# Kernel optimization log

Measured on AMD Instinct MI355X. Metric: run time of the kernel, lower is better.

## Reference

```python
import jax, jax.numpy as jnp
import numpy as np

B, QT, KT = 4, 1024, 1024
Q_SIZE, K_SIZE, EMB, HEADS = 1024, 1024, 1024, 8
HEAD_DIM = EMB // HEADS


def setup_inputs() -> dict:
    key = jax.random.key(0)
    ks = jax.random.split(key, 8)
    query = jax.random.normal(ks[0], (B, QT, Q_SIZE), dtype=jnp.float32)
    key_t = jax.random.normal(ks[1], (B, KT, K_SIZE), dtype=jnp.float32)
    mask = jax.random.randint(ks[2], (B, QT, KT), 0, 2, dtype=jnp.int32)
    # Linear weights stored as (in, out); torch Linear computes x @ W.T, equivalent here.
    sq = 1.0 / np.sqrt(Q_SIZE)
    sk = 1.0 / np.sqrt(K_SIZE)
    se = 1.0 / np.sqrt(EMB)
    Wq = jax.random.uniform(ks[3], (Q_SIZE, EMB), jnp.float32, -sq, sq)
    Wk = jax.random.uniform(ks[4], (K_SIZE, EMB), jnp.float32, -sk, sk)
    Wv = jax.random.uniform(ks[5], (K_SIZE, EMB), jnp.float32, -sk, sk)
    Wu = jax.random.uniform(ks[6], (EMB, EMB), jnp.float32, -se, se)
    bu = jax.random.uniform(ks[7], (EMB,), jnp.float32, -se, se)
    return {"query": query, "key": key_t, "mask": mask,
            "Wq": Wq, "Wk": Wk, "Wv": Wv, "Wu": Wu, "bu": bu}


def reference(query, key, mask, Wq, Wk, Wv, Wu, bu):
    b, q_t, _ = query.shape
    k_t = key.shape[1]
    q = (query @ Wq).reshape(b, q_t, HEADS, HEAD_DIM)   # b i n d
    k = (key @ Wk).reshape(b, k_t, HEADS, HEAD_DIM)     # b j n d
    v = (key @ Wv).reshape(b, k_t, HEADS, HEAD_DIM)
    # NOTE: original module defines self.scale but never applies it.
    att_score = jnp.einsum('bind,bjnd->bijn', q, k)
    att_score = jnp.where(mask[..., None] == 0, jnp.float32(-1e9), att_score)
    att_prob = jax.nn.softmax(att_score, axis=2)        # softmax over key axis j
    att_vec = jnp.einsum('bijn,bjnd->bind', att_prob, v).reshape(b, q_t, EMB)
    return att_vec @ Wu + bu
```

## Files before the change

kernel.cpp:

```cpp
#include <hip/hip_runtime.h>
#include <hip/hip_bf16.h>


typedef __attribute__((ext_vector_type(8))) short bf16x8;
typedef __attribute__((ext_vector_type(4))) float f32x4;

static constexpr int BB = 4;
static constexpr int TT = 1024;
static constexpr int EE = 1024;
static constexpr int HH = 8;
static constexpr int DD = 128;

static __device__ __forceinline__ unsigned short f2b(float x) {
  union { float f; unsigned int u; } c; c.f = x;
  unsigned int r = c.u + 0x7fffu + ((c.u >> 16) & 1u);
  return (unsigned short)(r >> 16);
}

static __device__ __forceinline__ unsigned int cvtpk(float lo, float hi) {
  unsigned int r;
  asm("v_cvt_pk_bf16_f32 %0, %1, %2" : "=v"(r) : "v"(lo), "v"(hi));
  return r;
}

static __device__ __forceinline__ float exp2x(float x) {
  float r;
  asm("v_exp_f32 %0, %1" : "=v"(r) : "v"(x));
  return r;
}

static __device__ __forceinline__ void gload_lds16(const void* g, void* l) {
  __builtin_amdgcn_global_load_lds(
      (const __attribute__((address_space(1))) unsigned int*)g,
      (__attribute__((address_space(3))) unsigned int*)l, 16, 0, 0);
}

__global__ __launch_bounds__(256) void cvt_kernel(
    const float* __restrict__ qf, const float* __restrict__ kf,
    unsigned short* __restrict__ qb, unsigned short* __restrict__ kb) {
  int i = blockIdx.x * 256 + threadIdx.x;
  float4 a = ((const float4*)qf)[i];
  ushort4 oa; oa.x = f2b(a.x); oa.y = f2b(a.y); oa.z = f2b(a.z); oa.w = f2b(a.w);
  ((ushort4*)qb)[i] = oa;
  float4 b = ((const float4*)kf)[i];
  ushort4 ob; ob.x = f2b(b.x); ob.y = f2b(b.y); ob.z = f2b(b.z); ob.w = f2b(b.w);
  ((ushort4*)kb)[i] = ob;
}

struct WT4 { const float* src[4]; unsigned short* dst[4]; float scale[4]; };

__global__ __launch_bounds__(256) void wtrans_kernel(WT4 wt) {
  const float* src = wt.src[blockIdx.z];
  unsigned short* dst = wt.dst[blockIdx.z];
  const float sc = wt.scale[blockIdx.z];
  __shared__ float tile[32][33];
  int n0 = blockIdx.x * 32, k0 = blockIdx.y * 32;
  int tx = threadIdx.x, ty = threadIdx.y;
#pragma unroll
  for (int i = 0; i < 4; ++i)
    tile[ty + i * 8][tx] = src[(size_t)(k0 + ty + i * 8) * EE + n0 + tx];
  __syncthreads();
#pragma unroll
  for (int i = 0; i < 4; ++i)
    dst[(size_t)(n0 + ty + i * 8) * EE + k0 + tx] = f2b(tile[tx][ty + i * 8] * sc);
}

__global__ __launch_bounds__(256) void vtrans_kernel(
    const unsigned short* __restrict__ vp, unsigned short* __restrict__ vt) {
  int bh = blockIdx.z; int b = bh >> 3, h = bh & 7;
  int d0 = blockIdx.x * 32, kt0 = blockIdx.y * 32;
  __shared__ unsigned short tile[32][33];
  int tx = threadIdx.x, ty = threadIdx.y;
#pragma unroll
  for (int i = 0; i < 4; ++i)
    tile[ty + i * 8][tx] =
        vp[(size_t)(b * TT + kt0 + ty + i * 8) * EE + h * DD + d0 + tx];
  __syncthreads();
#pragma unroll
  for (int i = 0; i < 4; ++i)
    vt[(size_t)((b * HH + h) * DD + d0 + ty + i * 8) * TT + kt0 + tx] =
        tile[tx][ty + i * 8];
}

__global__ __launch_bounds__(256) void maskpack_kernel(
    const int* __restrict__ mask, unsigned long long* __restrict__ mbits) {
  int row = blockIdx.x * 4 + (threadIdx.x >> 6);
  int lane = threadIdx.x & 63;
  const int* mrow = mask + (size_t)row * TT;
  unsigned long long myw = 0;
#pragma unroll
  for (int jw = 0; jw < 16; ++jw) {
    unsigned long long bal = __ballot(mrow[jw * 64 + lane] != 0);
    if (lane == jw) myw = bal;
  }
  if (lane < 16) mbits[(size_t)row * 16 + lane] = myw;
}

static __device__ __forceinline__ void gemm_core(
    const unsigned short* __restrict__ A, const unsigned short* __restrict__ Bt,
    unsigned short* __restrict__ Cb) {
  constexpr int K = EE, N = EE;
  __shared__ __align__(16) unsigned short As[128 * 32];
  __shared__ __align__(16) unsigned short Bs[128 * 32];
  const int tid = threadIdx.x, lane = tid & 63, w = tid >> 6;
  const int wm = w >> 1, wn = w & 1;
  const int bm = blockIdx.x, bn = blockIdx.y;
  const int g4 = lane >> 4, l15 = lane & 15;
  const int srow = lane >> 2;
  const int scol = (lane & 3) * 8;

  f32x4 acc[4][4] = {};

  for (int kt = 0; kt < K / 32; ++kt) {
    const int k0 = kt * 32;
#pragma unroll
    for (int it = 0; it < 2; ++it) {
      int r = it * 64 + w * 16;
      gload_lds16(A + (size_t)(bm * 128 + r + srow) * K + k0 + scol, As + r * 32);
      gload_lds16(Bt + (size_t)(bn * 128 + r + srow) * K + k0 + scol, Bs + r * 32);
    }
    __syncthreads();
    bf16x8 af[4], bf[4];
#pragma unroll
    for (int i = 0; i < 4; ++i) {
      af[i] = *(const bf16x8*)(As + (wm * 64 + i * 16 + l15) * 32 + g4 * 8);
      bf[i] = *(const bf16x8*)(Bs + (wn * 64 + i * 16 + l15) * 32 + g4 * 8);
    }
#pragma unroll
    for (int i = 0; i < 4; ++i)
#pragma unroll
      for (int j = 0; j < 4; ++j)
        acc[i][j] = __builtin_amdgcn_mfma_f32_16x16x32_bf16(af[i], bf[j],
                                                            acc[i][j], 0, 0, 0);
    __syncthreads();
  }

  const int rr = g4 * 4;
#pragma unroll
  for (int i = 0; i < 4; ++i)
#pragma unroll
    for (int j = 0; j < 4; ++j) {
      int row = bm * 128 + wm * 64 + i * 16 + rr;
      int col = bn * 128 + wn * 64 + j * 16 + l15;
#pragma unroll
      for (int r = 0; r < 4; ++r)
        Cb[(size_t)(row + r) * N + col] = f2b(acc[i][j][r]);
    }
}

struct Gemm3 { const unsigned short* A[3]; const unsigned short* Bt[3];
               unsigned short* C[3]; };

__global__ __launch_bounds__(256) void proj_gemm_kernel(Gemm3 g) {
  int z = blockIdx.z;
  gemm_core(g.A[z], g.Bt[z], g.C[z]);
}

__global__ __launch_bounds__(256) void out_gemm_kernel(
    const unsigned short* __restrict__ A, const unsigned short* __restrict__ Bt,
    float* __restrict__ Cf, const float* __restrict__ bias) {
  constexpr int K = EE, N = EE;
  __shared__ __align__(16) unsigned short As[64 * 32];
  __shared__ __align__(16) unsigned short Bs[128 * 32];
  const int tid = threadIdx.x, lane = tid & 63, w = tid >> 6;
  const int wm = w >> 1, wn = w & 1;
  const int bm = blockIdx.x, bn = blockIdx.y;
  const int g4 = lane >> 4, l15 = lane & 15;

  f32x4 acc[2][4] = {};

  for (int kt = 0; kt < K / 32; ++kt) {
    const int k0 = kt * 32;
    {
      int row = tid >> 2, c = tid & 3;
      gload_lds16(A + (size_t)(bm * 64 + row) * K + k0 + c * 8, As + tid * 8);
    }
#pragma unroll
    for (int it = 0; it < 2; ++it) {
      int idx = it * 256 + tid;
      int row = idx >> 2, c = idx & 3;
      gload_lds16(Bt + (size_t)(bn * 128 + row) * K + k0 + c * 8, Bs + idx * 8);
    }
    __syncthreads();
    bf16x8 af[2], bf[4];
#pragma unroll
    for (int i = 0; i < 2; ++i)
      af[i] = *(const bf16x8*)(As + (wm * 32 + i * 16 + l15) * 32 + g4 * 8);
#pragma unroll
    for (int j = 0; j < 4; ++j)
      bf[j] = *(const bf16x8*)(Bs + (wn * 64 + j * 16 + l15) * 32 + g4 * 8);
#pragma unroll
    for (int i = 0; i < 2; ++i)
#pragma unroll
      for (int j = 0; j < 4; ++j)
        acc[i][j] = __builtin_amdgcn_mfma_f32_16x16x32_bf16(af[i], bf[j],
                                                            acc[i][j], 0, 0, 0);
    __syncthreads();
  }

  const int rr = g4 * 4;
#pragma unroll
  for (int i = 0; i < 2; ++i)
#pragma unroll
    for (int j = 0; j < 4; ++j) {
      int row = bm * 64 + wm * 32 + i * 16 + rr;
      int col = bn * 128 + wn * 64 + j * 16 + l15;
#pragma unroll
      for (int r = 0; r < 4; ++r)
        Cf[(size_t)(row + r) * N + col] = acc[i][j][r] + bias[col];
    }
}

__global__ __launch_bounds__(256) void attn_kernel(
    const unsigned short* __restrict__ q, const unsigned short* __restrict__ k,
    const unsigned short* __restrict__ vt,
    const unsigned long long* __restrict__ mbits,
    unsigned short* __restrict__ av) {
  extern __shared__ __align__(16) char smem[];

  const int tid = threadIdx.x, lane = tid & 63, w = tid >> 6;
  const int orig = blockIdx.x + 16 * blockIdx.y + 128 * blockIdx.z;
  const int qt = (orig >> 3) & 15;
  const int pair = ((orig & 7) << 2) | (orig >> 7);
  const int h = pair & 7, b = pair >> 3;
  const int i0 = qt * 64 + w * 16;
  const int g4 = lane >> 4, l15 = lane & 15;
  const int swz = (l15 & 7) << 4;

  bf16x8 aq[4];
  {
    const unsigned short* qb =
        q + (size_t)(b * TT + i0 + l15) * EE + h * DD + g4 * 8;
#pragma unroll
    for (int kc = 0; kc < 4; ++kc) aq[kc] = *(const bf16x8*)(qb + kc * 32);
  }

  const unsigned short* kb0 = k + (size_t)(b * TT) * EE + h * DD;
  const unsigned short* vb0 = vt + (size_t)((b * HH + h) * DD) * TT;
  const unsigned short* kptr[4];
  const unsigned short* vptr[4];
  int chunkb[4];
#pragma unroll
  for (int p = 0; p < 4; ++p) {
    int base = p * 256 + w * 64;
    int idx = base + lane;
    int kr = idx >> 4, kcc = (idx & 15) ^ (kr & 7);
    kptr[p] = kb0 + (size_t)kr * EE + kcc * 8;
    int vr = idx >> 3, vcc = (idx & 7) ^ (vr & 7);
    vptr[p] = vb0 + (size_t)vr * TT + vcc * 8;
    chunkb[p] = base * 16;
  }

  const unsigned long long* mb = mbits + ((size_t)(b * TT + i0 + l15) << 4);
  unsigned long long mcur = mb[0];

  int kb_[4], vb_[2];
#pragma unroll
  for (int kc = 0; kc < 4; ++kc)
    kb_[kc] = l15 * 256 + ((kc * 64 + g4 * 16) ^ swz);
#pragma unroll
  for (int h2 = 0; h2 < 2; ++h2)
    vb_[h2] = 32768 + l15 * 128 + ((h2 * 64 + g4 * 16) ^ swz);

#pragma unroll
  for (int p = 0; p < 4; ++p) {
    gload_lds16(kptr[p], smem + chunkb[p]);
    gload_lds16(vptr[p], smem + 32768 + chunkb[p]);
  }
#pragma unroll
  for (int p = 0; p < 4; ++p) { kptr[p] += 64 * EE; vptr[p] += 64; }

  f32x4 oacc[8] = {};
  float mrun = -__builtin_inff(), lrun = 0.f;

  __syncthreads();
  int bufoff = 0;

  for (int t = 0; t < 16; ++t) {
    unsigned long long mnext = 0;
    if (t < 15) {
      mnext = mb[t + 1];
      int dst = bufoff ^ 16384;
#pragma unroll
      for (int p = 0; p < 4; ++p) {
        gload_lds16(kptr[p], smem + dst + chunkb[p]);
        gload_lds16(vptr[p], smem + 32768 + dst + chunkb[p]);
      }
#pragma unroll
      for (int p = 0; p < 4; ++p) { kptr[p] += 64 * EE; vptr[p] += 64; }
    }

    f32x4 sacc[4] = {};
    __builtin_amdgcn_s_setprio(1);
#pragma unroll
    for (int kc = 0; kc < 4; ++kc)
#pragma unroll
      for (int nt = 0; nt < 4; ++nt) {
        bf16x8 bk = *(const bf16x8*)(smem + kb_[kc] + nt * 4096);
        sacc[nt] = __builtin_amdgcn_mfma_f32_16x16x32_bf16(bk, aq[kc],
                                                           sacc[nt], 0, 0, 0);
      }
    __builtin_amdgcn_s_setprio(0);

    {
      unsigned int wlo = (unsigned int)mcur, whi = (unsigned int)(mcur >> 32);
#pragma unroll
      for (int nt = 0; nt < 4; ++nt) {
        unsigned int ww = (nt < 2) ? wlo : whi;
        int bb = (nt & 1) * 16 + g4 * 4;
#pragma unroll
        for (int r = 0; r < 4; ++r)
          if (((ww >> (bb + r)) & 1u) == 0u) sacc[nt][r] = -1e9f;
      }
    }

    float mx = sacc[0][0];
#pragma unroll
    for (int nt = 0; nt < 4; ++nt)
#pragma unroll
      for (int r = 0; r < 4; ++r) mx = fmaxf(mx, sacc[nt][r]);
    mx = fmaxf(mx, __shfl_xor(mx, 16, 64));
    mx = fmaxf(mx, __shfl_xor(mx, 32, 64));

    if (__any(mx > mrun + 8.f)) {
      float mnew = fmaxf(mrun, mx);
      float sc = exp2x(mrun - mnew);
      lrun *= sc;
      mrun = mnew;
      float scO[4];
#pragma unroll
      for (int r = 0; r < 4; ++r)
        scO[r] = __shfl(sc, (lane & 48) | (((lane & 48) >> 2) + r), 64);
#pragma unroll
      for (int dt = 0; dt < 8; ++dt)
#pragma unroll
        for (int r = 0; r < 4; ++r) oacc[dt][r] *= scO[r];
    }

    float p[4][4];
    float s0 = 0.f;
#pragma unroll
    for (int nt = 0; nt < 4; ++nt)
#pragma unroll
      for (int r = 0; r < 4; ++r) {
        float pv = exp2x(sacc[nt][r] - mrun);
        p[nt][r] = pv;
        s0 += pv;
      }
    s0 += __shfl_xor(s0, 16, 64);
    s0 += __shfl_xor(s0, 32, 64);
    lrun += s0;

    unsigned int paw[2][4];
#pragma unroll
    for (int h2 = 0; h2 < 2; ++h2) {
      unsigned int D0a = cvtpk(p[2 * h2][0], p[2 * h2][1]);
      unsigned int D1a = cvtpk(p[2 * h2][2], p[2 * h2][3]);
      unsigned int D0b = cvtpk(p[2 * h2 + 1][0], p[2 * h2 + 1][1]);
      unsigned int D1b = cvtpk(p[2 * h2 + 1][2], p[2 * h2 + 1][3]);
      unsigned int r1 = __shfl_xor(g4 < 2 ? D0a : D0b, 16, 64);
      unsigned int r2 = __shfl_xor(g4 < 2 ? D1a : D1b, 16, 64);
      unsigned int r3 = __shfl_xor(g4 == 0 ? D0b : D0a, 32, 64);
      unsigned int r4 = __shfl_xor(g4 == 0 ? D1b : D1a, 32, 64);
      unsigned int r5 = __shfl_xor(g4 == 2 ? D0a : D0b, 48, 64);
      unsigned int r6 = __shfl_xor(g4 == 2 ? D1a : D1b, 48, 64);
      paw[h2][0] = g4 == 0 ? D0a : g4 == 1 ? r5 : g4 == 2 ? r3 : r1;
      paw[h2][1] = g4 == 0 ? D1a : g4 == 1 ? r6 : g4 == 2 ? r4 : r2;
      paw[h2][2] = g4 == 0 ? r1 : g4 == 1 ? r3 : g4 == 2 ? r5 : D0b;
      paw[h2][3] = g4 == 0 ? r2 : g4 == 1 ? r4 : g4 == 2 ? r6 : D1b;
    }

    __builtin_amdgcn_s_setprio(1);
#pragma unroll
    for (int h2 = 0; h2 < 2; ++h2) {
      union { unsigned int u[4]; bf16x8 v; } pau;
      pau.u[0] = paw[h2][0]; pau.u[1] = paw[h2][1];
      pau.u[2] = paw[h2][2]; pau.u[3] = paw[h2][3];
#pragma unroll
      for (int dt = 0; dt < 8; ++dt) {
        bf16x8 bv = *(const bf16x8*)(smem + vb_[h2] + dt * 2048);
        oacc[dt] = __builtin_amdgcn_mfma_f32_16x16x32_bf16(pau.v, bv, oacc[dt],
                                                           0, 0, 0);
      }
    }
    __builtin_amdgcn_s_setprio(0);

    __syncthreads();
    bufoff ^= 16384;
#pragma unroll
    for (int kc = 0; kc < 4; ++kc) kb_[kc] ^= 16384;
#pragma unroll
    for (int h2 = 0; h2 < 2; ++h2) vb_[h2] ^= 16384;
    mcur = mnext;
  }

  float linv[4];
#pragma unroll
  for (int r = 0; r < 4; ++r)
    linv[r] = 1.f / __shfl(lrun, (lane & 48) | (((lane & 48) >> 2) + r), 64);
  unsigned short* ob =
      av + (size_t)(b * TT + i0 + g4 * 4) * EE + h * DD + l15;
#pragma unroll
  for (int dt = 0; dt < 8; ++dt)
#pragma unroll
    for (int r = 0; r < 4; ++r)
      ob[(size_t)r * EE + dt * 16] = f2b(oacc[dt][r] * linv[r]);
}

extern "C" void kernel_launch(void* const* d_in, const int* in_sizes, int n_in,
                              void* d_out, int out_size, void* d_ws,
                              size_t ws_size, hipStream_t stream) {
  const float* query = (const float*)d_in[0];
  const float* key   = (const float*)d_in[1];
  const int*   mask  = (const int*)d_in[2];
  const float* Wq    = (const float*)d_in[3];
  const float* Wk    = (const float*)d_in[4];
  const float* Wv    = (const float*)d_in[5];
  const float* Wu    = (const float*)d_in[6];
  const float* bu    = (const float*)d_in[7];
  float* out = (float*)d_out;

  char* ws = (char*)d_ws;
  const size_t MB = 1024 * 1024;
  unsigned short* qbf = (unsigned short*)(ws);
  unsigned short* kbf = (unsigned short*)(ws + 8 * MB);
  unsigned short* Wqt = (unsigned short*)(ws + 16 * MB);
  unsigned short* Wkt = (unsigned short*)(ws + 18 * MB);
  unsigned short* Wvt = (unsigned short*)(ws + 20 * MB);
  unsigned short* Wut = (unsigned short*)(ws + 22 * MB);
  unsigned short* qp  = (unsigned short*)(ws + 24 * MB);
  unsigned short* kp  = (unsigned short*)(ws + 32 * MB);
  unsigned short* vp  = (unsigned short*)(ws + 40 * MB);
  unsigned short* vtb = (unsigned short*)(ws + 48 * MB);
  unsigned short* av  = (unsigned short*)(ws + 56 * MB);
  unsigned long long* mbt = (unsigned long long*)(ws + 40 * MB);

  cvt_kernel<<<4096, 256, 0, stream>>>(query, key, qbf, kbf);

  WT4 wt; wt.src[0] = Wq; wt.src[1] = Wk; wt.src[2] = Wv; wt.src[3] = Wu;
  wt.dst[0] = Wqt; wt.dst[1] = Wkt; wt.dst[2] = Wvt; wt.dst[3] = Wut;
  wt.scale[0] = 1.4426950408889634f;
  wt.scale[1] = 1.0f; wt.scale[2] = 1.0f; wt.scale[3] = 1.0f;
  wtrans_kernel<<<dim3(32, 32, 4), dim3(32, 8), 0, stream>>>(wt);

  Gemm3 g3;
  g3.A[0] = qbf; g3.A[1] = kbf; g3.A[2] = kbf;
  g3.Bt[0] = Wqt; g3.Bt[1] = Wkt; g3.Bt[2] = Wvt;
  g3.C[0] = qp; g3.C[1] = kp; g3.C[2] = vp;
  proj_gemm_kernel<<<dim3(32, 8, 3), 256, 0, stream>>>(g3);

  vtrans_kernel<<<dim3(4, 32, 32), dim3(32, 8), 0, stream>>>(vp, vtb);

  maskpack_kernel<<<1024, 256, 0, stream>>>(mask, mbt);

  attn_kernel<<<dim3(16, 8, 4), 256, 65536, stream>>>(qp, kp, vtb, mbt, av);

  out_gemm_kernel<<<dim3(64, 8), 256, 0, stream>>>(av, Wut, out, bu);
}
```

Measured before the change: 119.4 us.

## Load V fragments directly to registers in attention; widen projection GEMM K-tile with swizzle

The attention kernel stops staging V through shared memory. Each wave now loads its V^T MFMA operands straight from global memory into registers at the start of every key tile. This halves the dynamic LDS to 32 KB and adds a launch-bounds hint of 2 blocks per CU for higher occupancy, at the cost of more VGPRs and uncoalesced, redundantly fetched global V loads. Separately, the projection GEMM moves to a 64-wide K tile with an XOR-swizzled LDS layout, which halves the barrier count and reduces bank conflicts.

```diff
diff --git a/kernel.cpp b/kernel.cpp
--- a/kernel.cpp
+++ b/kernel.cpp
@@ -100,38 +100,43 @@
     const unsigned short* __restrict__ A, const unsigned short* __restrict__ Bt,
     unsigned short* __restrict__ Cb) {
   constexpr int K = EE, N = EE;
-  __shared__ __align__(16) unsigned short As[128 * 32];
-  __shared__ __align__(16) unsigned short Bs[128 * 32];
+  __shared__ __align__(16) unsigned short As[128 * 64];
+  __shared__ __align__(16) unsigned short Bs[128 * 64];
   const int tid = threadIdx.x, lane = tid & 63, w = tid >> 6;
   const int wm = w >> 1, wn = w & 1;
   const int bm = blockIdx.x, bn = blockIdx.y;
   const int g4 = lane >> 4, l15 = lane & 15;
-  const int srow = lane >> 2;
-  const int scol = (lane & 3) * 8;
 
   f32x4 acc[4][4] = {};
 
-  for (int kt = 0; kt < K / 32; ++kt) {
-    const int k0 = kt * 32;
-#pragma unroll
-    for (int it = 0; it < 2; ++it) {
-      int r = it * 64 + w * 16;
-      gload_lds16(A + (size_t)(bm * 128 + r + srow) * K + k0 + scol, As + r * 32);
-      gload_lds16(Bt + (size_t)(bn * 128 + r + srow) * K + k0 + scol, Bs + r * 32);
+  for (int kt = 0; kt < K / 64; ++kt) {
+    const int k0 = kt * 64;
+#pragma unroll
+    for (int it = 0; it < 4; ++it) {
+      int idx = it * 256 + tid;
+      int r = idx >> 3, c = (idx & 7) ^ (r & 7);
+      gload_lds16(A + (size_t)(bm * 128 + r) * K + k0 + c * 8, As + idx * 8);
+      gload_lds16(Bt + (size_t)(bn * 128 + r) * K + k0 + c * 8, Bs + idx * 8);
     }
     __syncthreads();
-    bf16x8 af[4], bf[4];
-#pragma unroll
-    for (int i = 0; i < 4; ++i) {
-      af[i] = *(const bf16x8*)(As + (wm * 64 + i * 16 + l15) * 32 + g4 * 8);
-      bf[i] = *(const bf16x8*)(Bs + (wn * 64 + i * 16 + l15) * 32 + g4 * 8);
-    }
-#pragma unroll
-    for (int i = 0; i < 4; ++i)
-#pragma unroll
-      for (int j = 0; j < 4; ++j)
-        acc[i][j] = __builtin_amdgcn_mfma_f32_16x16x32_bf16(af[i], bf[j],
-                                                            acc[i][j], 0, 0, 0);
+    bf16x8 af[2][4], bf[2][4];
+#pragma unroll
+    for (int kc2 = 0; kc2 < 2; ++kc2) {
+      int co = ((kc2 * 4 + g4) ^ (l15 & 7)) * 8;
+#pragma unroll
+      for (int i = 0; i < 4; ++i) {
+        af[kc2][i] = *(const bf16x8*)(As + (wm * 64 + i * 16 + l15) * 64 + co);
+        bf[kc2][i] = *(const bf16x8*)(Bs + (wn * 64 + i * 16 + l15) * 64 + co);
+      }
+    }
+#pragma unroll
+    for (int kc2 = 0; kc2 < 2; ++kc2)
+#pragma unroll
+      for (int i = 0; i < 4; ++i)
+#pragma unroll
+        for (int j = 0; j < 4; ++j)
+          acc[i][j] = __builtin_amdgcn_mfma_f32_16x16x32_bf16(
+              af[kc2][i], bf[kc2][j], acc[i][j], 0, 0, 0);
     __syncthreads();
   }
 
@@ -211,7 +216,7 @@
     }
 }
 
-__global__ __launch_bounds__(256) void attn_kernel(
+__global__ __launch_bounds__(256, 2) void attn_kernel(
     const unsigned short* __restrict__ q, const unsigned short* __restrict__ k,
     const unsigned short* __restrict__ vt,
     const unsigned long long* __restrict__ mbits,
@@ -236,9 +241,7 @@
   }
 
   const unsigned short* kb0 = k + (size_t)(b * TT) * EE + h * DD;
-  const unsigned short* vb0 = vt + (size_t)((b * HH + h) * DD) * TT;
   const unsigned short* kptr[4];
-  const unsigned short* vptr[4];
   int chunkb[4];
 #pragma unroll
   for (int p = 0; p < 4; ++p) {
@@ -246,29 +249,24 @@
     int idx = base + lane;
     int kr = idx >> 4, kcc = (idx & 15) ^ (kr & 7);
     kptr[p] = kb0 + (size_t)kr * EE + kcc * 8;
-    int vr = idx >> 3, vcc = (idx & 7) ^ (vr & 7);
-    vptr[p] = vb0 + (size_t)vr * TT + vcc * 8;
     chunkb[p] = base * 16;
   }
+
+  const unsigned short* vfb =
+      vt + (size_t)((b * HH + h) * DD + l15) * TT + g4 * 8;
 
   const unsigned long long* mb = mbits + ((size_t)(b * TT + i0 + l15) << 4);
   unsigned long long mcur = mb[0];
 
-  int kb_[4], vb_[2];
+  int kb_[4];
 #pragma unroll
   for (int kc = 0; kc < 4; ++kc)
     kb_[kc] = l15 * 256 + ((kc * 64 + g4 * 16) ^ swz);
-#pragma unroll
-  for (int h2 = 0; h2 < 2; ++h2)
-    vb_[h2] = 32768 + l15 * 128 + ((h2 * 64 + g4 * 16) ^ swz);
-
-#pragma unroll
-  for (int p = 0; p < 4; ++p) {
-    gload_lds16(kptr[p], smem + chunkb[p]);
-    gload_lds16(vptr[p], smem + 32768 + chunkb[p]);
-  }
-#pragma unroll
-  for (int p = 0; p < 4; ++p) { kptr[p] += 64 * EE; vptr[p] += 64; }
+
+#pragma unroll
+  for (int p = 0; p < 4; ++p) gload_lds16(kptr[p], smem + chunkb[p]);
+#pragma unroll
+  for (int p = 0; p < 4; ++p) kptr[p] += 64 * EE;
 
   f32x4 oacc[8] = {};
   float mrun = -__builtin_inff(), lrun = 0.f;
@@ -277,17 +275,26 @@
   int bufoff = 0;
 
   for (int t = 0; t < 16; ++t) {
+    bf16x8 vr[2][8];
+    {
+      const unsigned short* vtt = vfb + t * 64;
+#pragma unroll
+      for (int h2 = 0; h2 < 2; ++h2)
+#pragma unroll
+        for (int dt = 0; dt < 8; ++dt)
+          vr[h2][dt] =
+              *(const bf16x8*)(vtt + (size_t)dt * 16 * TT + h2 * 32);
+    }
+
     unsigned long long mnext = 0;
     if (t < 15) {
       mnext = mb[t + 1];
       int dst = bufoff ^ 16384;
 #pragma unroll
-      for (int p = 0; p < 4; ++p) {
+      for (int p = 0; p < 4; ++p)
         gload_lds16(kptr[p], smem + dst + chunkb[p]);
-        gload_lds16(vptr[p], smem + 32768 + dst + chunkb[p]);
-      }
-#pragma unroll
-      for (int p = 0; p < 4; ++p) { kptr[p] += 64 * EE; vptr[p] += 64; }
+#pragma unroll
+      for (int p = 0; p < 4; ++p) kptr[p] += 64 * EE;
     }
 
     f32x4 sacc[4] = {};
@@ -377,11 +384,9 @@
       pau.u[0] = paw[h2][0]; pau.u[1] = paw[h2][1];
       pau.u[2] = paw[h2][2]; pau.u[3] = paw[h2][3];
 #pragma unroll
-      for (int dt = 0; dt < 8; ++dt) {
-        bf16x8 bv = *(const bf16x8*)(smem + vb_[h2] + dt * 2048);
-        oacc[dt] = __builtin_amdgcn_mfma_f32_16x16x32_bf16(pau.v, bv, oacc[dt],
-                                                           0, 0, 0);
-      }
+      for (int dt = 0; dt < 8; ++dt)
+        oacc[dt] = __builtin_amdgcn_mfma_f32_16x16x32_bf16(
+            pau.v, vr[h2][dt], oacc[dt], 0, 0, 0);
     }
     __builtin_amdgcn_s_setprio(0);
 
@@ -389,8 +394,6 @@
     bufoff ^= 16384;
 #pragma unroll
     for (int kc = 0; kc < 4; ++kc) kb_[kc] ^= 16384;
-#pragma unroll
-    for (int h2 = 0; h2 < 2; ++h2) vb_[h2] ^= 16384;
     mcur = mnext;
   }
 
@@ -453,7 +456,7 @@
 
   maskpack_kernel<<<1024, 256, 0, stream>>>(mask, mbt);
 
-  attn_kernel<<<dim3(16, 8, 4), 256, 65536, stream>>>(qp, kp, vtb, mbt, av);
+  attn_kernel<<<dim3(16, 8, 4), 256, 32768, stream>>>(qp, kp, vtb, mbt, av);
 
   out_gemm_kernel<<<dim3(64, 8), 256, 0, stream>>>(av, Wut, out, bu);
 }
```

Result: slower. 151.2 us (+26.6%).

## Deepen GEMM K-tile with XOR swizzle and relax attention loop barrier placement

Applied to the files above, without the earlier changes.

The projection GEMM now stages 64-wide K tiles instead of 32, halving the number of barrier pairs per K loop. It uses an XOR-swizzled LDS layout so the wider rows do not cause bank conflicts on the fragment reads. In the attention loop, the end-of-iteration __syncthreads is replaced by a bare s_barrier at the start of the next iteration plus an explicit vmcnt wait that lets the prefetch of the next K/V tile stay in flight. The hand-written waitcnt/barrier ordering is fragile: if the vmcnt count does not match the number of outstanding loads, data races on the double buffer could appear.

```diff
diff --git a/kernel.cpp b/kernel.cpp
--- a/kernel.cpp
+++ b/kernel.cpp
@@ -100,38 +100,43 @@
     const unsigned short* __restrict__ A, const unsigned short* __restrict__ Bt,
     unsigned short* __restrict__ Cb) {
   constexpr int K = EE, N = EE;
-  __shared__ __align__(16) unsigned short As[128 * 32];
-  __shared__ __align__(16) unsigned short Bs[128 * 32];
+  __shared__ __align__(16) unsigned short As[128 * 64];
+  __shared__ __align__(16) unsigned short Bs[128 * 64];
   const int tid = threadIdx.x, lane = tid & 63, w = tid >> 6;
   const int wm = w >> 1, wn = w & 1;
   const int bm = blockIdx.x, bn = blockIdx.y;
   const int g4 = lane >> 4, l15 = lane & 15;
-  const int srow = lane >> 2;
-  const int scol = (lane & 3) * 8;
 
   f32x4 acc[4][4] = {};
 
-  for (int kt = 0; kt < K / 32; ++kt) {
-    const int k0 = kt * 32;
-#pragma unroll
-    for (int it = 0; it < 2; ++it) {
-      int r = it * 64 + w * 16;
-      gload_lds16(A + (size_t)(bm * 128 + r + srow) * K + k0 + scol, As + r * 32);
-      gload_lds16(Bt + (size_t)(bn * 128 + r + srow) * K + k0 + scol, Bs + r * 32);
+  for (int kt = 0; kt < K / 64; ++kt) {
+    const int k0 = kt * 64;
+#pragma unroll
+    for (int it = 0; it < 4; ++it) {
+      int idx = it * 256 + tid;
+      int r = idx >> 3, c = (idx & 7) ^ (r & 7);
+      gload_lds16(A + (size_t)(bm * 128 + r) * K + k0 + c * 8, As + idx * 8);
+      gload_lds16(Bt + (size_t)(bn * 128 + r) * K + k0 + c * 8, Bs + idx * 8);
     }
     __syncthreads();
-    bf16x8 af[4], bf[4];
-#pragma unroll
-    for (int i = 0; i < 4; ++i) {
-      af[i] = *(const bf16x8*)(As + (wm * 64 + i * 16 + l15) * 32 + g4 * 8);
-      bf[i] = *(const bf16x8*)(Bs + (wn * 64 + i * 16 + l15) * 32 + g4 * 8);
-    }
-#pragma unroll
-    for (int i = 0; i < 4; ++i)
-#pragma unroll
-      for (int j = 0; j < 4; ++j)
-        acc[i][j] = __builtin_amdgcn_mfma_f32_16x16x32_bf16(af[i], bf[j],
-                                                            acc[i][j], 0, 0, 0);
+    bf16x8 af[2][4], bf[2][4];
+#pragma unroll
+    for (int kc2 = 0; kc2 < 2; ++kc2) {
+      int co = ((kc2 * 4 + g4) ^ (l15 & 7)) * 8;
+#pragma unroll
+      for (int i = 0; i < 4; ++i) {
+        af[kc2][i] = *(const bf16x8*)(As + (wm * 64 + i * 16 + l15) * 64 + co);
+        bf[kc2][i] = *(const bf16x8*)(Bs + (wn * 64 + i * 16 + l15) * 64 + co);
+      }
+    }
+#pragma unroll
+    for (int kc2 = 0; kc2 < 2; ++kc2)
+#pragma unroll
+      for (int i = 0; i < 4; ++i)
+#pragma unroll
+        for (int j = 0; j < 4; ++j)
+          acc[i][j] = __builtin_amdgcn_mfma_f32_16x16x32_bf16(
+              af[kc2][i], bf[kc2][j], acc[i][j], 0, 0, 0);
     __syncthreads();
   }
 
@@ -277,6 +282,8 @@
   int bufoff = 0;
 
   for (int t = 0; t < 16; ++t) {
+    if (t > 0) __builtin_amdgcn_s_barrier();
+
     unsigned long long mnext = 0;
     if (t < 15) {
       mnext = mb[t + 1];
@@ -288,6 +295,11 @@
       }
 #pragma unroll
       for (int p = 0; p < 4; ++p) { kptr[p] += 64 * EE; vptr[p] += 64; }
+      asm volatile("s_waitcnt vmcnt(8)" ::: "memory");
+      __builtin_amdgcn_sched_barrier(0);
+    } else {
+      asm volatile("s_waitcnt vmcnt(0)" ::: "memory");
+      __builtin_amdgcn_sched_barrier(0);
     }
 
     f32x4 sacc[4] = {};
@@ -385,7 +397,6 @@
     }
     __builtin_amdgcn_s_setprio(0);
 
-    __syncthreads();
     bufoff ^= 16384;
 #pragma unroll
     for (int kc = 0; kc < 4; ++kc) kb_[kc] ^= 16384;
```

Result: no change. 118.0 us (-1.2%).
